# Kernel tuning notes

Hardware: AMD Instinct MI355X
Metric: run time of the kernel (lower is better)

Reference implementation:

```python
import jax, jax.numpy as jnp
import numpy as np

N = 100000   # nodes
E = 1600000  # edges
NC = 10000   # candidates
G = 1000     # graphs
ND = 32      # node_emb_dim
ED = 8       # edge_emb_dim
L = 4        # num_layers


def setup_inputs() -> dict:
    key = jax.random.key(0)
    ks = jax.random.split(key, 12)
    s = 0.1
    return {
        "x": jax.random.normal(ks[0], (N, 2), dtype=jnp.float32),
        "edge_attr": jax.random.normal(ks[1], (E, 1), dtype=jnp.float32),
        "Wn_in": jax.random.normal(ks[2], (2, ND)) * s,
        "bn_in": jnp.zeros((ND,)),
        "We_in": jax.random.normal(ks[3], (1, ED)) * s,
        "be_in": jnp.zeros((ED,)),
        "We_l": jax.random.normal(ks[4], (L, 2 * ND + ED, ED)) * s,
        "be_l": jnp.zeros((L, ED)),
        "Wn_l": jax.random.normal(ks[5], (L, ND + ED, ND)) * s,
        "bn_l": jnp.zeros((L, ND)),
        "Wout": jax.random.normal(ks[6], (ND, 1)) * s,
        "bout": jnp.zeros((1,)),
        "edge_index": jax.random.randint(ks[7], (2, E), 0, N),
        "batch": jnp.sort(jax.random.randint(ks[8], (N,), 0, G)),
        "candidate_idxs": jax.random.randint(ks[9], (NC,), 0, N),
    }


def reference(x, edge_attr, Wn_in, bn_in, We_in, be_in, We_l, be_l, Wn_l, bn_l,
              Wout, bout, edge_index, batch, candidate_idxs):
    h = x @ Wn_in + bn_in            # [N, ND]
    e = edge_attr @ We_in + be_in    # [E, ED]
    src, dst = edge_index[0], edge_index[1]
    for l in range(L):
        # edge update: MLP on [x_src, x_dst, edge_attr]
        m = jnp.concatenate([h[src], h[dst], e], axis=-1)        # [E, 2*ND+ED]
        new_e = jax.nn.relu(m @ We_l[l] + be_l[l])               # [E, ED]
        # aggregate (aggr='add') messages at destination nodes
        agg = jax.ops.segment_sum(new_e, dst, num_segments=N)    # [N, ED]
        new_h = jax.nn.relu(jnp.concatenate([h, agg], axis=-1) @ Wn_l[l] + bn_l[l])
        h = h + new_h   # residual
        e = e + new_e   # residual
    logits = (h[candidate_idxs] @ Wout + bout)[:, 0]             # [NC]
    seg = batch[candidate_idxs]                                  # [NC] graph ids
    # scatter_log_softmax over per-graph candidate groups
    mx = jax.ops.segment_max(logits, seg, num_segments=G)
    shifted = logits - mx[seg]
    lse = jnp.log(jax.ops.segment_sum(jnp.exp(shifted), seg, num_segments=G))
    return shifted - lse[seg]
```

## Files before the change

kernel.cpp:

```cpp
#include <hip/hip_runtime.h>

#define ND 32
#define ED 8
#define NL 4
#define NG 1000
#define NBC_MAX 512
#define CHUNK 8192
#define CHUNK_H 4096
#define NBLK 64

typedef unsigned short u16;

__device__ __forceinline__ int xcd_swizzle(int b, int nb) {
  int per = nb >> 3;
  return (b < (per << 3)) ? ((b & 7) * per + (b >> 3)) : b;
}


__device__ __forceinline__ u16 f2bf(float f) {
  unsigned u = __float_as_uint(f);
  u += 0x7fffu + ((u >> 16) & 1u);
  return (u16)(u >> 16);
}
__device__ __forceinline__ unsigned pack2(float a, float b) {
  return (unsigned)f2bf(a) | ((unsigned)f2bf(b) << 16);
}
__device__ __forceinline__ void cvt8(uint4 p, float* o) {
  o[0] = __uint_as_float(p.x << 16); o[1] = __uint_as_float(p.x & 0xffff0000u);
  o[2] = __uint_as_float(p.y << 16); o[3] = __uint_as_float(p.y & 0xffff0000u);
  o[4] = __uint_as_float(p.z << 16); o[5] = __uint_as_float(p.z & 0xffff0000u);
  o[6] = __uint_as_float(p.w << 16); o[7] = __uint_as_float(p.w & 0xffff0000u);
}
__device__ __forceinline__ uint4 pack8(const float* v) {
  uint4 o;
  o.x = pack2(v[0], v[1]); o.y = pack2(v[2], v[3]);
  o.z = pack2(v[4], v[5]); o.w = pack2(v[6], v[7]);
  return o;
}


__global__ void k_init_h(const float* __restrict__ x,
                         const float* __restrict__ W,
                         const float* __restrict__ b,
                         const float* __restrict__ We,
                         const float* __restrict__ be,
                         u16* __restrict__ h,
                         u16* __restrict__ zs, u16* __restrict__ zd,
                         int N) {
  int n = xcd_swizzle(blockIdx.x, gridDim.x) * blockDim.x + threadIdx.x;
  if (n >= N) return;
  float x0 = x[2 * n], x1 = x[2 * n + 1];
  float v[ND];
#pragma unroll
  for (int d = 0; d < ND; ++d) v[d] = fmaf(x0, W[d], fmaf(x1, W[ND + d], b[d]));
#pragma unroll
  for (int d = 0; d < ND; ++d) v[d] = __uint_as_float((unsigned)f2bf(v[d]) << 16);
  uint4* h4 = reinterpret_cast<uint4*>(h + (size_t)n * ND);
#pragma unroll
  for (int q = 0; q < 4; ++q) h4[q] = pack8(&v[q * 8]);
  float zsv[ED], zdv[ED];
#pragma unroll
  for (int j = 0; j < ED; ++j) { zsv[j] = 0.0f; zdv[j] = be[j]; }
#pragma unroll
  for (int k = 0; k < ND; ++k)
#pragma unroll
    for (int j = 0; j < ED; ++j) {
      zsv[j] = fmaf(v[k], We[k * ED + j], zsv[j]);
      zdv[j] = fmaf(v[k], We[(ND + k) * ED + j], zdv[j]);
    }
  *reinterpret_cast<uint4*>(zs + (size_t)n * ED) = pack8(zsv);
  *reinterpret_cast<uint4*>(zd + (size_t)n * ED) = pack8(zdv);
}


__global__ void k_chist(const int* __restrict__ dst, int* __restrict__ bcnt,
                        int E, int nbc) {
  __shared__ int lcnt[NBC_MAX];
  for (int b = threadIdx.x; b < nbc; b += blockDim.x) lcnt[b] = 0;
  __syncthreads();
  int e0 = blockIdx.x * CHUNK_H;
  int e1 = min(e0 + CHUNK_H, E);
  for (int i = e0 + threadIdx.x; i < e1; i += blockDim.x)
    atomicAdd(&lcnt[dst[i] >> 8], 1);
  __syncthreads();
  for (int b = threadIdx.x; b < nbc; b += blockDim.x)
    if (lcnt[b]) atomicAdd(&bcnt[b], lcnt[b]);
}

__global__ void k_cscan(const int* __restrict__ bcnt, int* __restrict__ bbase,
                        int nbc) {
  __shared__ int s[NBC_MAX];
  int tid = threadIdx.x;
  if (nbc <= NBC_MAX) {
    int v = (tid < nbc) ? bcnt[tid] : 0;
    s[tid] = v;
    __syncthreads();
    for (int st = 1; st < NBC_MAX; st <<= 1) {
      int t = (tid >= st) ? s[tid - st] : 0;
      __syncthreads();
      s[tid] += t;
      __syncthreads();
    }
    if (tid < nbc) bbase[tid] = s[tid] - v;
    if (tid == nbc - 1) bbase[nbc] = s[tid];
  } else if (tid == 0) {
    int run = 0;
    for (int i = 0; i < nbc; ++i) { bbase[i] = run; run += bcnt[i]; }
    bbase[nbc] = run;
  }
}

__global__ void k_binA(const int* __restrict__ src, const int* __restrict__ dst,
                       const float* __restrict__ ea,
                       const int* __restrict__ bbase, int* __restrict__ cursor_c,
                       uint2* __restrict__ binned, int E, int nbc) {
  __shared__ int lcnt[NBC_MAX];
  __shared__ int lbase[NBC_MAX];
  for (int b = threadIdx.x; b < nbc; b += blockDim.x) lcnt[b] = 0;
  __syncthreads();
  int e0 = blockIdx.x * CHUNK;
  int e1 = min(e0 + CHUNK, E);
  for (int i = e0 + threadIdx.x; i < e1; i += blockDim.x)
    atomicAdd(&lcnt[dst[i] >> 8], 1);
  __syncthreads();
  for (int b = threadIdx.x; b < nbc; b += blockDim.x) {
    int c = lcnt[b];
    lbase[b] = c ? (bbase[b] + atomicAdd(&cursor_c[b], c)) : 0;
  }
  __syncthreads();
  for (int i = e0 + threadIdx.x; i < e1; i += blockDim.x) {
    int d = dst[i];
    int pos = atomicAdd(&lbase[d >> 8], 1);
    binned[pos] = make_uint2((unsigned)src[i] | ((unsigned)(d & 255) << 24),
                             __float_as_uint(ea[i]));
  }
}

__global__ void k_binB(const uint2* __restrict__ binned,
                       const int* __restrict__ bbase,
                       int* __restrict__ ssrc, float* __restrict__ ea_s,
                       int* __restrict__ noffs,
                       int N) {
  __shared__ int hist[256];
  __shared__ int scn[256];
  int b = blockIdx.x;
  int base = bbase[b], end = bbase[b + 1];
  int node0 = b << 8;
  int nn = min(256, N - node0);
  hist[threadIdx.x] = 0;
  __syncthreads();
  for (int p = base + threadIdx.x; p < end; p += blockDim.x)
    atomicAdd(&hist[binned[p].x >> 24], 1);
  __syncthreads();
  int v = hist[threadIdx.x];
  scn[threadIdx.x] = v;
  __syncthreads();
  for (int st = 1; st < 256; st <<= 1) {
    int t = (threadIdx.x >= (unsigned)st) ? scn[threadIdx.x - st] : 0;
    __syncthreads();
    scn[threadIdx.x] += t;
    __syncthreads();
  }
  int excl = base + scn[threadIdx.x] - v;
  if ((int)threadIdx.x < nn) noffs[node0 + threadIdx.x] = excl;
  if (threadIdx.x == 0) noffs[min(node0 + 256, N)] = end;
  hist[threadIdx.x] = excl;
  __syncthreads();
  for (int p = base + threadIdx.x; p < end; p += blockDim.x) {
    uint2 rec = binned[p];
    int dl = (int)(rec.x >> 24);
    int pos = atomicAdd(&hist[dl], 1);
    ssrc[pos] = (int)(rec.x & 0xffffffu);
    ea_s[pos] = __uint_as_float(rec.y);
  }
}

template <int L0>
__global__ void k_layer(u16* __restrict__ h,
                        u16* __restrict__ e,
                        const float* __restrict__ ea_s,
                        const int* __restrict__ ssrc,
                        const int* __restrict__ noffs,
                        const u16* __restrict__ zs,
                        const u16* __restrict__ zd,
                        const float* __restrict__ Wei,
                        const float* __restrict__ bei,
                        const float* __restrict__ W3,
                        const float* __restrict__ Wn,
                        const float* __restrict__ bn,
                        const float* __restrict__ Wen,
                        const float* __restrict__ ben,
                        u16* __restrict__ zs_n, u16* __restrict__ zd_n,
                        int N) {
  int n = xcd_swizzle(blockIdx.x, gridDim.x) * blockDim.x + threadIdx.x;
  if (n >= N) return;
  int o0 = noffs[n], o1 = noffs[n + 1];
  float zdv[ED];
  cvt8(*reinterpret_cast<const uint4*>(zd + (size_t)n * ED), zdv);
  float av[ED];
#pragma unroll
  for (int j = 0; j < ED; ++j) av[j] = 0.0f;
  for (int p = o0; p < o1; ++p) {
    int s = ssrc[p];
    float zsv[ED];
    cvt8(*reinterpret_cast<const uint4*>(zs + (size_t)s * ED), zsv);
    float ein[ED];
    if (L0) {
      float a = ea_s[p];
#pragma unroll
      for (int j = 0; j < ED; ++j) ein[j] = fmaf(a, Wei[j], bei[j]);
    } else {
      cvt8(*reinterpret_cast<const uint4*>(e + (size_t)p * ED), ein);
    }
    float acc[ED];
#pragma unroll
    for (int j = 0; j < ED; ++j) acc[j] = zsv[j] + zdv[j];
#pragma unroll
    for (int k = 0; k < ED; ++k)
#pragma unroll
      for (int j = 0; j < ED; ++j)
        acc[j] = fmaf(ein[k], W3[k * ED + j], acc[j]);
    float eo[ED];
#pragma unroll
    for (int j = 0; j < ED; ++j) {
      float r = fmaxf(acc[j], 0.0f);
      av[j] += r;
      eo[j] = ein[j] + r;
    }
    *reinterpret_cast<uint4*>(e + (size_t)p * ED) = pack8(eo);
  }
  float acc[ND];
#pragma unroll
  for (int j = 0; j < ND; ++j) acc[j] = bn[j];
  uint4* h4 = reinterpret_cast<uint4*>(h + (size_t)n * ND);
  float hv[ND];
#pragma unroll
  for (int q = 0; q < 4; ++q) cvt8(h4[q], &hv[q * 8]);
#pragma unroll
  for (int k = 0; k < ND; ++k)
#pragma unroll
    for (int j = 0; j < ND; ++j) acc[j] = fmaf(hv[k], Wn[k * ND + j], acc[j]);
#pragma unroll
  for (int k = 0; k < ED; ++k)
#pragma unroll
    for (int j = 0; j < ND; ++j) acc[j] = fmaf(av[k], Wn[(ND + k) * ND + j], acc[j]);
  float hn[ND];
#pragma unroll
  for (int k = 0; k < ND; ++k) {
    float o = hv[k] + fmaxf(acc[k], 0.0f);
    hn[k] = __uint_as_float((unsigned)f2bf(o) << 16);
  }
#pragma unroll
  for (int q = 0; q < 4; ++q) h4[q] = pack8(&hn[q * 8]);
  float zsv[ED], zdv2[ED];
#pragma unroll
  for (int j = 0; j < ED; ++j) { zsv[j] = 0.0f; zdv2[j] = ben[j]; }
#pragma unroll
  for (int k = 0; k < ND; ++k)
#pragma unroll
    for (int j = 0; j < ED; ++j) {
      zsv[j] = fmaf(hn[k], Wen[k * ED + j], zsv[j]);
      zdv2[j] = fmaf(hn[k], Wen[(ND + k) * ED + j], zdv2[j]);
    }
  *reinterpret_cast<uint4*>(zs_n + (size_t)n * ED) = pack8(zsv);
  *reinterpret_cast<uint4*>(zd_n + (size_t)n * ED) = pack8(zdv2);
}


__device__ __forceinline__ unsigned int enc_f32(float f) {
  unsigned int bits = __float_as_uint(f);
  return (bits & 0x80000000u) ? ~bits : (bits | 0x80000000u);
}
__device__ __forceinline__ float dec_f32(unsigned int u) {
  unsigned int bits = (u & 0x80000000u) ? (u ^ 0x80000000u) : ~u;
  return __uint_as_float(bits);
}

__global__ void k_cand(const u16* __restrict__ h,
                       const u16* __restrict__ e,
                       const u16* __restrict__ zs,
                       const u16* __restrict__ zd,
                       const int* __restrict__ ssrc,
                       const int* __restrict__ noffs,
                       const int* __restrict__ cand,
                       const int* __restrict__ batch,
                       const float* __restrict__ W3,
                       const float* __restrict__ Wn,
                       const float* __restrict__ bn,
                       const float* __restrict__ Wout,
                       const float* __restrict__ bout,
                       float* __restrict__ logits,
                       int* __restrict__ seg,
                       unsigned int* __restrict__ mxu,
                       int NC) {
  int c = blockIdx.x * blockDim.x + threadIdx.x;
  if (c >= NC) return;
  int n = cand[c];
  int o0 = noffs[n], o1 = noffs[n + 1];
  float zdv[ED];
  cvt8(*reinterpret_cast<const uint4*>(zd + (size_t)n * ED), zdv);
  float av[ED];
#pragma unroll
  for (int j = 0; j < ED; ++j) av[j] = 0.0f;
  for (int p = o0; p < o1; ++p) {
    int s = ssrc[p];
    float zsv[ED], ein[ED], acc[ED];
    cvt8(*reinterpret_cast<const uint4*>(zs + (size_t)s * ED), zsv);
    cvt8(*reinterpret_cast<const uint4*>(e + (size_t)p * ED), ein);
#pragma unroll
    for (int j = 0; j < ED; ++j) acc[j] = zsv[j] + zdv[j];
#pragma unroll
    for (int k = 0; k < ED; ++k)
#pragma unroll
      for (int j = 0; j < ED; ++j)
        acc[j] = fmaf(ein[k], W3[k * ED + j], acc[j]);
#pragma unroll
    for (int j = 0; j < ED; ++j) av[j] += fmaxf(acc[j], 0.0f);
  }
  float acc[ND];
#pragma unroll
  for (int j = 0; j < ND; ++j) acc[j] = bn[j];
  const uint4* h4 = reinterpret_cast<const uint4*>(h + (size_t)n * ND);
  float hv[ND];
#pragma unroll
  for (int q = 0; q < 4; ++q) cvt8(h4[q], &hv[q * 8]);
#pragma unroll
  for (int k = 0; k < ND; ++k)
#pragma unroll
    for (int j = 0; j < ND; ++j) acc[j] = fmaf(hv[k], Wn[k * ND + j], acc[j]);
#pragma unroll
  for (int k = 0; k < ED; ++k)
#pragma unroll
    for (int j = 0; j < ND; ++j) acc[j] = fmaf(av[k], Wn[(ND + k) * ND + j], acc[j]);
  float lg = bout[0];
#pragma unroll
  for (int k = 0; k < ND; ++k)
    lg = fmaf(hv[k] + fmaxf(acc[k], 0.0f), Wout[k], lg);
  logits[c] = lg;
  int g = batch[n];
  seg[c] = g;
  atomicMax(&mxu[g], enc_f32(lg));
}

__global__ void k_expsum(float* __restrict__ logits,
                         const int* __restrict__ seg,
                         const unsigned int* __restrict__ mxu,
                         float* __restrict__ sum,
                         int NC) {
  int c = blockIdx.x * blockDim.x + threadIdx.x;
  if (c >= NC) return;
  int g = seg[c];
  float sh = logits[c] - dec_f32(mxu[g]);
  logits[c] = sh;
  atomicAdd(&sum[g], expf(sh));
}

__global__ void k_final(const float* __restrict__ shifted,
                        const int* __restrict__ seg,
                        const float* __restrict__ sum,
                        float* __restrict__ out, int NC) {
  int c = blockIdx.x * blockDim.x + threadIdx.x;
  if (c >= NC) return;
  out[c] = shifted[c] - logf(sum[seg[c]]);
}


extern "C" void kernel_launch(void* const* d_in, const int* in_sizes, int n_in,
                              void* d_out, int out_size, void* d_ws, size_t ws_size,
                              hipStream_t stream) {
  const float* x       = (const float*)d_in[0];
  const float* ea      = (const float*)d_in[1];
  const float* Wn_in   = (const float*)d_in[2];
  const float* bn_in   = (const float*)d_in[3];
  const float* We_in   = (const float*)d_in[4];
  const float* be_in   = (const float*)d_in[5];
  const float* We_l    = (const float*)d_in[6];
  const float* be_l    = (const float*)d_in[7];
  const float* Wn_l    = (const float*)d_in[8];
  const float* bn_l    = (const float*)d_in[9];
  const float* Wout    = (const float*)d_in[10];
  const float* bout    = (const float*)d_in[11];
  const int* edge_index= (const int*)d_in[12];
  const int* batch     = (const int*)d_in[13];
  const int* cand      = (const int*)d_in[14];

  const int N  = in_sizes[13];
  const int E  = in_sizes[1];
  const int NC = in_sizes[14];
  const int nbc = (N + 255) >> 8;

  char* ws = (char*)d_ws;
  uint2* binned = (uint2*)ws; ws += (size_t)E * sizeof(uint2);
  int*   ssrc   = (int*)ws;   ws += (size_t)E * sizeof(int);
  float* ea_s   = (float*)ws; ws += (size_t)E * sizeof(float);
  u16*   h      = (u16*)ws;   ws += (size_t)N * ND * sizeof(u16);
  u16*   e      = (u16*)ws;   ws += (size_t)E * ED * sizeof(u16);
  u16*   zs0    = (u16*)ws;   ws += (size_t)N * ED * sizeof(u16);
  u16*   zd0    = (u16*)ws;   ws += (size_t)N * ED * sizeof(u16);
  u16*   zs1    = (u16*)ws;   ws += (size_t)N * ED * sizeof(u16);
  u16*   zd1    = (u16*)ws;   ws += (size_t)N * ED * sizeof(u16);
  int*   noffs  = (int*)ws;   ws += ((size_t)N + 4) * sizeof(int);
  int*   bcnt   = (int*)ws;   ws += (size_t)NBC_MAX * sizeof(int);
  int*   cursor = (int*)ws;   ws += (size_t)NBC_MAX * sizeof(int);
  int*   bbase  = (int*)ws;   ws += ((size_t)NBC_MAX + 4) * sizeof(int);
  float* logits = (float*)ws; ws += (size_t)NC * sizeof(float);
  int*   seg    = (int*)ws;   ws += (size_t)NC * sizeof(int);
  unsigned int* mxu = (unsigned int*)ws; ws += (size_t)NG * sizeof(unsigned int);
  float* sum    = (float*)ws; ws += (size_t)NG * sizeof(float);

  const int* srcp = edge_index;
  const int* dstp = edge_index + E;
  const int blk = 256;
  const size_t WE_STRIDE = (size_t)(2 * ND + ED) * ED;

  hipMemsetAsync(bcnt, 0, 2 * (size_t)NBC_MAX * sizeof(int), stream);
  k_chist<<<(E + CHUNK_H - 1) / CHUNK_H, 1024, 0, stream>>>(dstp, bcnt, E, nbc);
  k_cscan<<<1, NBC_MAX, 0, stream>>>(bcnt, bbase, nbc);
  k_binA<<<(E + CHUNK - 1) / CHUNK, 1024, 0, stream>>>(srcp, dstp, ea, bbase,
                                                       cursor, binned, E, nbc);
  k_binB<<<nbc, 256, 0, stream>>>(binned, bbase, ssrc, ea_s, noffs, N);

  k_init_h<<<(N + NBLK - 1) / NBLK, NBLK, 0, stream>>>(x, Wn_in, bn_in, We_l,
                                                       be_l, h, zs0, zd0, N);

  const int ngrid = (N + NBLK - 1) / NBLK;
  u16* zsc = zs0; u16* zdc = zd0;
  u16* zsn = zs1; u16* zdn = zd1;
  for (int l = 0; l < NL - 1; ++l) {
    const float* W3 = We_l + l * WE_STRIDE + (size_t)2 * ND * ED;
    const float* Wn = Wn_l + (size_t)l * (ND + ED) * ND;
    const float* bn = bn_l + (size_t)l * ND;
    const float* Wen = We_l + (l + 1) * WE_STRIDE;
    const float* ben = be_l + (size_t)(l + 1) * ED;
    if (l == 0) {
      k_layer<1><<<ngrid, NBLK, 0, stream>>>(
          h, e, ea_s, ssrc, noffs, zsc, zdc, We_in, be_in, W3, Wn, bn,
          Wen, ben, zsn, zdn, N);
    } else {
      k_layer<0><<<ngrid, NBLK, 0, stream>>>(
          h, e, ea_s, ssrc, noffs, zsc, zdc, We_in, be_in, W3, Wn, bn,
          Wen, ben, zsn, zdn, N);
    }
    u16* t;
    t = zsc; zsc = zsn; zsn = t;
    t = zdc; zdc = zdn; zdn = t;
  }

  hipMemsetAsync(mxu, 0, NG * (sizeof(unsigned int) + sizeof(float)), stream);
  {
    const int l = NL - 1;
    const float* W3 = We_l + l * WE_STRIDE + (size_t)2 * ND * ED;
    const float* Wn = Wn_l + (size_t)l * (ND + ED) * ND;
    const float* bn = bn_l + (size_t)l * ND;
    k_cand<<<(NC + NBLK - 1) / NBLK, NBLK, 0, stream>>>(
        h, e, zsc, zdc, ssrc, noffs, cand, batch, W3, Wn, bn, Wout, bout,
        logits, seg, mxu, NC);
  }
  k_expsum<<<(NC + blk - 1) / blk, blk, 0, stream>>>(logits, seg, mxu, sum, NC);
  k_final<<<(NC + blk - 1) / blk, blk, 0, stream>>>(logits, seg, sum,
                                                    (float*)d_out, NC);
}
```

Baseline: 365.8 us.

## Split per-node edge loops across thread groups with shuffle reductions

```diff
diff --git a/kernel.cpp b/kernel.cpp
--- a/kernel.cpp
+++ b/kernel.cpp
@@ -192,7 +192,9 @@
                         const float* __restrict__ ben,
                         u16* __restrict__ zs_n, u16* __restrict__ zd_n,
                         int N) {
-  int n = xcd_swizzle(blockIdx.x, gridDim.x) * blockDim.x + threadIdx.x;
+  int t = xcd_swizzle(blockIdx.x, gridDim.x) * blockDim.x + threadIdx.x;
+  int n = t >> 2;
+  int g = t & 3;
   if (n >= N) return;
   int o0 = noffs[n], o1 = noffs[n + 1];
   float zdv[ED];
@@ -200,7 +202,7 @@
   float av[ED];
 #pragma unroll
   for (int j = 0; j < ED; ++j) av[j] = 0.0f;
-  for (int p = o0; p < o1; ++p) {
+  for (int p = o0 + g; p < o1; p += 4) {
     int s = ssrc[p];
     float zsv[ED];
     cvt8(*reinterpret_cast<const uint4*>(zs + (size_t)s * ED), zsv);
@@ -229,41 +231,62 @@
     }
     *reinterpret_cast<uint4*>(e + (size_t)p * ED) = pack8(eo);
   }
-  float acc[ND];
-#pragma unroll
-  for (int j = 0; j < ND; ++j) acc[j] = bn[j];
+#pragma unroll
+  for (int j = 0; j < ED; ++j) {
+    av[j] += __shfl_xor(av[j], 1);
+    av[j] += __shfl_xor(av[j], 2);
+  }
   uint4* h4 = reinterpret_cast<uint4*>(h + (size_t)n * ND);
   float hv[ND];
 #pragma unroll
   for (int q = 0; q < 4; ++q) cvt8(h4[q], &hv[q * 8]);
+  const int j0 = g * 8;
+  float acc8[8];
+#pragma unroll
+  for (int jj = 0; jj < 8; ++jj) acc8[jj] = bn[j0 + jj];
 #pragma unroll
   for (int k = 0; k < ND; ++k)
 #pragma unroll
-    for (int j = 0; j < ND; ++j) acc[j] = fmaf(hv[k], Wn[k * ND + j], acc[j]);
+    for (int jj = 0; jj < 8; ++jj)
+      acc8[jj] = fmaf(hv[k], Wn[k * ND + j0 + jj], acc8[jj]);
 #pragma unroll
   for (int k = 0; k < ED; ++k)
 #pragma unroll
-    for (int j = 0; j < ND; ++j) acc[j] = fmaf(av[k], Wn[(ND + k) * ND + j], acc[j]);
-  float hn[ND];
-#pragma unroll
-  for (int k = 0; k < ND; ++k) {
-    float o = hv[k] + fmaxf(acc[k], 0.0f);
-    hn[k] = __uint_as_float((unsigned)f2bf(o) << 16);
-  }
-#pragma unroll
-  for (int q = 0; q < 4; ++q) h4[q] = pack8(&hn[q * 8]);
-  float zsv[ED], zdv2[ED];
-#pragma unroll
-  for (int j = 0; j < ED; ++j) { zsv[j] = 0.0f; zdv2[j] = ben[j]; }
-#pragma unroll
-  for (int k = 0; k < ND; ++k)
+    for (int jj = 0; jj < 8; ++jj)
+      acc8[jj] = fmaf(av[k], Wn[(ND + k) * ND + j0 + jj], acc8[jj]);
+  float hn8[8];
+#pragma unroll
+  for (int jj = 0; jj < 8; ++jj) {
+    float o = hv[j0 + jj] + fmaxf(acc8[jj], 0.0f);
+    hn8[jj] = __uint_as_float((unsigned)f2bf(o) << 16);
+  }
+  h4[g] = pack8(hn8);
+  float pz[2 * ED];
+#pragma unroll
+  for (int j = 0; j < 2 * ED; ++j) pz[j] = 0.0f;
+#pragma unroll
+  for (int kk = 0; kk < 8; ++kk) {
+    float hk = hn8[kk];
+    int krow = j0 + kk;
 #pragma unroll
     for (int j = 0; j < ED; ++j) {
-      zsv[j] = fmaf(hn[k], Wen[k * ED + j], zsv[j]);
-      zdv2[j] = fmaf(hn[k], Wen[(ND + k) * ED + j], zdv2[j]);
+      pz[j] = fmaf(hk, Wen[krow * ED + j], pz[j]);
+      pz[ED + j] = fmaf(hk, Wen[(ND + krow) * ED + j], pz[ED + j]);
     }
-  *reinterpret_cast<uint4*>(zs_n + (size_t)n * ED) = pack8(zsv);
-  *reinterpret_cast<uint4*>(zd_n + (size_t)n * ED) = pack8(zdv2);
+  }
+#pragma unroll
+  for (int j = 0; j < 2 * ED; ++j) {
+    pz[j] += __shfl_xor(pz[j], 1);
+    pz[j] += __shfl_xor(pz[j], 2);
+  }
+  if (g == 0) {
+    *reinterpret_cast<uint4*>(zs_n + (size_t)n * ED) = pack8(pz);
+  } else if (g == 1) {
+    float zdo[ED];
+#pragma unroll
+    for (int j = 0; j < ED; ++j) zdo[j] = pz[ED + j] + ben[j];
+    *reinterpret_cast<uint4*>(zd_n + (size_t)n * ED) = pack8(zdo);
+  }
 }
 
 
@@ -293,7 +316,8 @@
                        int* __restrict__ seg,
                        unsigned int* __restrict__ mxu,
                        int NC) {
-  int c = blockIdx.x * blockDim.x + threadIdx.x;
+  int t = blockIdx.x * blockDim.x + threadIdx.x;
+  int c = t >> 3, g = t & 7;
   if (c >= NC) return;
   int n = cand[c];
   int o0 = noffs[n], o1 = noffs[n + 1];
@@ -302,7 +326,7 @@
   float av[ED];
 #pragma unroll
   for (int j = 0; j < ED; ++j) av[j] = 0.0f;
-  for (int p = o0; p < o1; ++p) {
+  for (int p = o0 + g; p < o1; p += 8) {
     int s = ssrc[p];
     float zsv[ED], ein[ED], acc[ED];
     cvt8(*reinterpret_cast<const uint4*>(zs + (size_t)s * ED), zsv);
@@ -317,29 +341,44 @@
 #pragma unroll
     for (int j = 0; j < ED; ++j) av[j] += fmaxf(acc[j], 0.0f);
   }
-  float acc[ND];
-#pragma unroll
-  for (int j = 0; j < ND; ++j) acc[j] = bn[j];
+#pragma unroll
+  for (int j = 0; j < ED; ++j) {
+    av[j] += __shfl_xor(av[j], 1);
+    av[j] += __shfl_xor(av[j], 2);
+    av[j] += __shfl_xor(av[j], 4);
+  }
   const uint4* h4 = reinterpret_cast<const uint4*>(h + (size_t)n * ND);
   float hv[ND];
 #pragma unroll
   for (int q = 0; q < 4; ++q) cvt8(h4[q], &hv[q * 8]);
+  const int j0 = g * 4;
+  float acc4[4];
+#pragma unroll
+  for (int jj = 0; jj < 4; ++jj) acc4[jj] = bn[j0 + jj];
 #pragma unroll
   for (int k = 0; k < ND; ++k)
 #pragma unroll
-    for (int j = 0; j < ND; ++j) acc[j] = fmaf(hv[k], Wn[k * ND + j], acc[j]);
+    for (int jj = 0; jj < 4; ++jj)
+      acc4[jj] = fmaf(hv[k], Wn[k * ND + j0 + jj], acc4[jj]);
 #pragma unroll
   for (int k = 0; k < ED; ++k)
 #pragma unroll
-    for (int j = 0; j < ND; ++j) acc[j] = fmaf(av[k], Wn[(ND + k) * ND + j], acc[j]);
-  float lg = bout[0];
-#pragma unroll
-  for (int k = 0; k < ND; ++k)
-    lg = fmaf(hv[k] + fmaxf(acc[k], 0.0f), Wout[k], lg);
-  logits[c] = lg;
-  int g = batch[n];
-  seg[c] = g;
-  atomicMax(&mxu[g], enc_f32(lg));
+    for (int jj = 0; jj < 4; ++jj)
+      acc4[jj] = fmaf(av[k], Wn[(ND + k) * ND + j0 + jj], acc4[jj]);
+  float lg = 0.0f;
+#pragma unroll
+  for (int jj = 0; jj < 4; ++jj)
+    lg = fmaf(hv[j0 + jj] + fmaxf(acc4[jj], 0.0f), Wout[j0 + jj], lg);
+  lg += __shfl_xor(lg, 1);
+  lg += __shfl_xor(lg, 2);
+  lg += __shfl_xor(lg, 4);
+  if (g == 0) {
+    lg += bout[0];
+    logits[c] = lg;
+    int gr = batch[n];
+    seg[c] = gr;
+    atomicMax(&mxu[gr], enc_f32(lg));
+  }
 }
 
 __global__ void k_expsum(float* __restrict__ logits,
@@ -423,7 +462,7 @@
   k_init_h<<<(N + NBLK - 1) / NBLK, NBLK, 0, stream>>>(x, Wn_in, bn_in, We_l,
                                                        be_l, h, zs0, zd0, N);
 
-  const int ngrid = (N + NBLK - 1) / NBLK;
+  const int ngrid4 = (N + 63) / 64;
   u16* zsc = zs0; u16* zdc = zd0;
   u16* zsn = zs1; u16* zdn = zd1;
   for (int l = 0; l < NL - 1; ++l) {
@@ -433,11 +472,11 @@
     const float* Wen = We_l + (l + 1) * WE_STRIDE;
     const float* ben = be_l + (size_t)(l + 1) * ED;
     if (l == 0) {
-      k_layer<1><<<ngrid, NBLK, 0, stream>>>(
+      k_layer<1><<<ngrid4, 256, 0, stream>>>(
           h, e, ea_s, ssrc, noffs, zsc, zdc, We_in, be_in, W3, Wn, bn,
           Wen, ben, zsn, zdn, N);
     } else {
-      k_layer<0><<<ngrid, NBLK, 0, stream>>>(
+      k_layer<0><<<ngrid4, 256, 0, stream>>>(
           h, e, ea_s, ssrc, noffs, zsc, zdc, We_in, be_in, W3, Wn, bn,
           Wen, ben, zsn, zdn, N);
     }
@@ -452,7 +491,7 @@
     const float* W3 = We_l + l * WE_STRIDE + (size_t)2 * ND * ED;
     const float* Wn = Wn_l + (size_t)l * (ND + ED) * ND;
     const float* bn = bn_l + (size_t)l * ND;
-    k_cand<<<(NC + NBLK - 1) / NBLK, NBLK, 0, stream>>>(
+    k_cand<<<((size_t)NC * 8 + 255) / 256, 256, 0, stream>>>(
         h, e, zsc, zdc, ssrc, noffs, cand, batch, W3, Wn, bn, Wout, bout,
         logits, seg, mxu, NC);
   }
```

New measurement: 372.2 us. No clear change (+1.8%).
